# Kernel tuning notes

Measured on AMD Instinct MI355X. Metric: run time of the kernel, lower is better.

## Reference

```python
import jax, jax.numpy as jnp
import numpy as np

B, C, H, W, L = 2, 64, 48, 48, 48
GH, GW, GL = 24, 24, 24  # gating signal at half resolution


def setup_inputs() -> dict:
    key = jax.random.key(0)
    k = jax.random.split(key, 6)
    x = jax.random.normal(k[0], (B, C, H, W, L), dtype=jnp.float32)
    g = jax.random.normal(k[1], (B, C, GH, GW, GL), dtype=jnp.float32)
    s = 1.0 / np.sqrt(C)
    W1 = jax.random.normal(k[2], (C, C), dtype=jnp.float32) * s  # conv1 1x1x1 weight (out,in)
    b1 = jax.random.normal(k[3], (C,), dtype=jnp.float32) * 0.01
    W2 = jax.random.normal(k[4], (C, C), dtype=jnp.float32) * s  # conv2 1x1x1 weight
    b2 = jax.random.normal(k[5], (C,), dtype=jnp.float32) * 0.01
    return {"x": x, "g": g, "W1": W1, "b1": b1, "W2": W2, "b2": b2}


def _conv1x1(v, Wm, b):
    # 1x1x1 Conv3d == channel-mixing matmul
    return jnp.einsum('bchwl,oc->bohwl', v, Wm) + b[None, :, None, None, None]


def reference(x, g, W1, b1, W2, b2):
    theta_x = _conv1x1(x, W1, b1)                       # (B, C, H, W, L)
    theta_g = _conv1x1(g, W2, b2)                       # (B, C, GH, GW, GL)
    # F.upsample(mode='trilinear', align_corners=False) -> half-pixel trilinear resize
    theta_g = jax.image.resize(theta_g, (B, C, H, W, L), method='trilinear')

    # spatially-normalized elementwise gate
    theta_c = theta_x * theta_g
    theta_c = theta_c - jnp.min(theta_c)                # global min over whole tensor
    theta_c = theta_c / jnp.sum(theta_c, axis=(2, 3, 4), keepdims=True)
    p = theta_c * x

    # channel-channel attention per (b,h,w), contracting over L
    theta_c_d = jnp.einsum('bihwl,bjhwl->bhwij', theta_x, theta_g)  # (B,H,W,C,C)
    theta_c_d = theta_c_d - jnp.min(theta_c_d)
    theta_c_d = theta_c_d / jnp.sum(theta_c_d, axis=(1, 2, 3, 4), keepdims=True)
    d = jnp.einsum('bchwl,bhwcj->bjhwl', x, theta_c_d)  # (B, C, H, W, L)
    return (p, d)
```

## Files before the change

### kernel.cpp

```cpp
#include <hip/hip_runtime.h>

#define Bb 2
#define Cc 64
#define Hh 48
#define Ww 48
#define Ll 48
#define HWc (Hh*Ww)
#define HWL (HWc*Ll)
#define GHh 24
#define SG (GHh*GHh*GHh)
#define NBLK (Bb*HWc)
#define CNT1f 110592.0f
#define CNT2f 9437184.0f

__device__ __forceinline__ void interp1(int i, int& a, int& b, float& f){
  float src = i*0.5f - 0.25f;
  float fl = floorf(src);
  f = src - fl;
  int i0 = (int)fl;
  a = i0 < 0 ? 0 : i0;
  int i1 = i0 + 1;
  b = i1 > (GHh-1) ? (GHh-1) : i1;
}

__global__ __launch_bounds__(256) void conv_k(const float* __restrict__ in,
    const float* __restrict__ Wm, const float* __restrict__ bias,
    float* __restrict__ out, int S){
  __shared__ __align__(16) float Wl[64][68];
  __shared__ __align__(16) float xl[64][68];
  int t = threadIdx.x;
  int ntile = S >> 6;
  int b  = blockIdx.x / ntile;
  int s0 = (blockIdx.x % ntile) << 6;
  for (int q = t; q < 4096; q += 256){
    int o = q >> 6, c = q & 63;
    Wl[c][o] = Wm[q];
  }
  const float* inb = in + (size_t)b*Cc*S + s0;
  for (int q = t; q < 1024; q += 256){
    int c = q >> 4, v = (q & 15) << 2;
    float4 val = *(const float4*)(inb + (size_t)c*S + v);
    *(float4*)&xl[c][v] = val;
  }
  __syncthreads();
  int o0 = (t & 15) << 2, s1 = (t >> 4) << 2;
  float a00=0,a01=0,a02=0,a03=0,a10=0,a11=0,a12=0,a13=0;
  float a20=0,a21=0,a22=0,a23=0,a30=0,a31=0,a32=0,a33=0;
  #pragma unroll 8
  for (int c = 0; c < 64; ++c){
    float4 wv = *(const float4*)&Wl[c][o0];
    float4 xv = *(const float4*)&xl[c][s1];
    a00 += wv.x*xv.x; a01 += wv.x*xv.y; a02 += wv.x*xv.z; a03 += wv.x*xv.w;
    a10 += wv.y*xv.x; a11 += wv.y*xv.y; a12 += wv.y*xv.z; a13 += wv.y*xv.w;
    a20 += wv.z*xv.x; a21 += wv.z*xv.y; a22 += wv.z*xv.z; a23 += wv.z*xv.w;
    a30 += wv.w*xv.x; a31 += wv.w*xv.y; a32 += wv.w*xv.z; a33 += wv.w*xv.w;
  }
  float* ob = out + (size_t)b*Cc*S + s0 + s1;
  float b0 = bias[o0+0], b1v = bias[o0+1], b2v = bias[o0+2], b3 = bias[o0+3];
  { float4 r = make_float4(a00+b0,a01+b0,a02+b0,a03+b0); *(float4*)(ob + (size_t)(o0+0)*S) = r; }
  { float4 r = make_float4(a10+b1v,a11+b1v,a12+b1v,a13+b1v); *(float4*)(ob + (size_t)(o0+1)*S) = r; }
  { float4 r = make_float4(a20+b2v,a21+b2v,a22+b2v,a23+b2v); *(float4*)(ob + (size_t)(o0+2)*S) = r; }
  { float4 r = make_float4(a30+b3,a31+b3,a32+b3,a33+b3); *(float4*)(ob + (size_t)(o0+3)*S) = r; }
}

__global__ __launch_bounds__(256) void upsample_k(const float* __restrict__ tgh,
    float* __restrict__ tg){
  __shared__ float shm[2][24][25];
  int t = threadIdx.x;
  int bc = blockIdx.x / Hh;
  int h  = blockIdx.x % Hh;
  int ha, hb; float fh; interp1(h, ha, hb, fh);
  const float* src = tgh + (size_t)bc*SG;
  for (int q = t; q < 288; q += 256){
    int p = q / 144, rem = q % 144;
    int w_ = rem / 6, vl = (rem % 6) << 2;
    int hs = p ? hb : ha;
    float4 v = *(const float4*)(src + (size_t)hs*576 + w_*24 + vl);
    shm[p][w_][vl+0]=v.x; shm[p][w_][vl+1]=v.y; shm[p][w_][vl+2]=v.z; shm[p][w_][vl+3]=v.w;
  }
  __syncthreads();
  float* dst = tg + ((size_t)bc*Hh + h)*HWc;
  float omf = 1.f - fh;
  #pragma unroll
  for (int k = 0; k < 9; ++k){
    int idx = t + (k << 8);
    int w = idx / 48, l = idx % 48;
    int wa, wb; float fw; interp1(w, wa, wb, fw);
    int la, lb; float fl; interp1(l, la, lb, fl);
    float vaa = omf*shm[0][wa][la] + fh*shm[1][wa][la];
    float vab = omf*shm[0][wa][lb] + fh*shm[1][wa][lb];
    float vba = omf*shm[0][wb][la] + fh*shm[1][wb][la];
    float vbb = omf*shm[0][wb][lb] + fh*shm[1][wb][lb];
    float va = (1.f-fw)*vaa + fw*vba;
    float vb = (1.f-fw)*vab + fw*vbb;
    dst[idx] = (1.f-fl)*va + fl*vb;
  }
}

__global__ __launch_bounds__(256) void reduce_k(const float* __restrict__ tx,
    const float* __restrict__ tg, float* __restrict__ part_row,
    float* __restrict__ pm1, float* __restrict__ pm2, float* __restrict__ ps2){
  __shared__ __align__(16) float txt[48][68];
  __shared__ __align__(16) float tgt[48][68];
  __shared__ float red[512];
  __shared__ float sxg[48];
  int t = threadIdx.x;
  int bIdx = blockIdx.x;
  int b = bIdx / HWc, hw = bIdx % HWc;
  const float* txb = tx + ((size_t)b*Cc*HWc + hw)*Ll;
  const float* tgb = tg + ((size_t)b*Cc*HWc + hw)*Ll;
  for (int q = t; q < 768; q += 256){
    int c = q / 12, v = (q % 12) << 2;
    float4 a = *(const float4*)(txb + (size_t)c*HWL + v);
    txt[v+0][c]=a.x; txt[v+1][c]=a.y; txt[v+2][c]=a.z; txt[v+3][c]=a.w;
    float4 g = *(const float4*)(tgb + (size_t)c*HWL + v);
    tgt[v+0][c]=g.x; tgt[v+1][c]=g.y; tgt[v+2][c]=g.z; tgt[v+3][c]=g.w;
  }
  __syncthreads();
  int c = t & 63, lg = t >> 6;
  float psum = 0.f, pmin = 3.4e38f;
  #pragma unroll
  for (int li = 0; li < 12; ++li){
    int l = lg*12 + li;
    float prod = txt[l][c]*tgt[l][c];
    psum += prod;
    pmin = fminf(pmin, prod);
  }
  red[t] = psum;
  if (t < 48){
    float sx = 0.f, sg = 0.f;
    #pragma unroll 8
    for (int cc = 0; cc < 64; ++cc){ sx += txt[t][cc]; sg += tgt[t][cc]; }
    sxg[t] = sx*sg;
  }
  __syncthreads();
  if (t < 64) part_row[(size_t)bIdx*64 + t] = red[t]+red[t+64]+red[t+128]+red[t+192];
  int i0 = (t & 15) << 2, j0 = (t >> 4) << 2;
  float a00=0,a01=0,a02=0,a03=0,a10=0,a11=0,a12=0,a13=0;
  float a20=0,a21=0,a22=0,a23=0,a30=0,a31=0,a32=0,a33=0;
  #pragma unroll 4
  for (int l = 0; l < 48; ++l){
    float4 av = *(const float4*)&txt[l][i0];
    float4 bv = *(const float4*)&tgt[l][j0];
    a00 += av.x*bv.x; a01 += av.x*bv.y; a02 += av.x*bv.z; a03 += av.x*bv.w;
    a10 += av.y*bv.x; a11 += av.y*bv.y; a12 += av.y*bv.z; a13 += av.y*bv.w;
    a20 += av.z*bv.x; a21 += av.z*bv.y; a22 += av.z*bv.z; a23 += av.z*bv.w;
    a30 += av.w*bv.x; a31 += av.w*bv.y; a32 += av.w*bv.z; a33 += av.w*bv.w;
  }
  float amin = fminf(fminf(fminf(a00,a01),fminf(a02,a03)),
               fminf(fminf(fminf(a10,a11),fminf(a12,a13)),
               fminf(fminf(fminf(a20,a21),fminf(a22,a23)),
                     fminf(fminf(a30,a31),fminf(a32,a33)))));
  __syncthreads();
  red[t] = pmin; red[256+t] = amin;
  __syncthreads();
  if (t < 128){
    red[t] = fminf(red[t], red[t+128]);
    red[256+t] = fminf(red[256+t], red[256+t+128]);
  }
  __syncthreads();
  if (t < 64){
    float v1 = fminf(red[t], red[t+64]);
    float v2 = fminf(red[256+t], red[256+t+64]);
    #pragma unroll
    for (int off = 32; off; off >>= 1){
      v1 = fminf(v1, __shfl_down(v1, off));
      v2 = fminf(v2, __shfl_down(v2, off));
    }
    if (t == 0){
      pm1[bIdx] = v1; pm2[bIdx] = v2;
      float tot = 0.f;
      #pragma unroll
      for (int l = 0; l < 48; ++l) tot += sxg[l];
      ps2[bIdx] = tot;
    }
  }
}

__global__ __launch_bounds__(256) void reduce2_k(const float* __restrict__ part_row,
    const float* __restrict__ pm1, const float* __restrict__ pm2,
    const float* __restrict__ ps2, float* __restrict__ rowsum,
    float* __restrict__ gmin, float* __restrict__ s2v){
  __shared__ float red[512];
  int t = threadIdx.x, blk = blockIdx.x;
  if (blk < 128){
    int b = blk >> 6, c = blk & 63;
    const float* src = part_row + (size_t)b*HWc*64 + c;
    float s = 0.f;
    #pragma unroll
    for (int k = 0; k < 9; ++k){
      int i = t + (k << 8);
      s += src[(size_t)i*64];
    }
    red[t] = s; __syncthreads();
    for (int sgap = 128; sgap >= 64; sgap >>= 1){
      if (t < sgap) red[t] += red[t+sgap];
      __syncthreads();
    }
    if (t < 64){
      float v = red[t];
      #pragma unroll
      for (int off = 32; off; off >>= 1) v += __shfl_down(v, off);
      if (t == 0) rowsum[blk] = v;
    }
  } else if (blk == 128){
    float m1 = 3.4e38f, m2 = 3.4e38f;
    for (int i = t; i < NBLK; i += 256){ m1 = fminf(m1, pm1[i]); m2 = fminf(m2, pm2[i]); }
    red[t] = m1; red[256+t] = m2; __syncthreads();
    for (int s = 128; s >= 1; s >>= 1){
      if (t < s){ red[t] = fminf(red[t], red[t+s]); red[256+t] = fminf(red[256+t], red[256+t+s]); }
      __syncthreads();
    }
    if (t == 0){ gmin[0] = red[0]; gmin[1] = red[256]; }
  } else {
    float sa = 0.f, sb = 0.f;
    for (int i = t; i < HWc; i += 256){ sa += ps2[i]; sb += ps2[HWc + i]; }
    red[t] = sa; red[256+t] = sb; __syncthreads();
    for (int s = 128; s >= 1; s >>= 1){
      if (t < s){ red[t] += red[t+s]; red[256+t] += red[256+t+s]; }
      __syncthreads();
    }
    if (t == 0){ s2v[0] = red[0]; s2v[1] = red[256]; }
  }
}

__global__ __launch_bounds__(256) void final_k(const float* __restrict__ x,
    const float* __restrict__ tx, const float* __restrict__ tg,
    const float* __restrict__ gmin, const float* __restrict__ rowsum,
    const float* __restrict__ s2v, float* __restrict__ outp, float* __restrict__ outd){
  __shared__ __align__(16) float sh[6528 + 3328 + 48 + 64];
  float* txt = sh;
  float* tgt = sh + 3264;
  float* At  = sh;
  float* xs  = sh + 6528;
  float* Xs  = sh + 6528 + 3328;
  float* iv1 = Xs + 48;
  int t = threadIdx.x;
  int bIdx = blockIdx.x;
  int b = bIdx / HWc, hw = bIdx % HWc;
  size_t sbase = ((size_t)b*Cc*HWc + hw)*Ll;
  const float* txb = tx + sbase;
  const float* tgb = tg + sbase;
  const float* xb  = x  + sbase;
  for (int q = t; q < 768; q += 256){
    int c = q / 12, v = (q % 12) << 2;
    float4 a = *(const float4*)(txb + (size_t)c*HWL + v);
    txt[(v+0)*68+c]=a.x; txt[(v+1)*68+c]=a.y; txt[(v+2)*68+c]=a.z; txt[(v+3)*68+c]=a.w;
    float4 g = *(const float4*)(tgb + (size_t)c*HWL + v);
    tgt[(v+0)*68+c]=g.x; tgt[(v+1)*68+c]=g.y; tgt[(v+2)*68+c]=g.z; tgt[(v+3)*68+c]=g.w;
    float4 xv = *(const float4*)(xb + (size_t)c*HWL + v);
    *(float4*)&xs[c*52 + v] = xv;
  }
  __syncthreads();
  if (t < 48){
    float s = 0.f;
    #pragma unroll 8
    for (int cc = 0; cc < 64; ++cc) s += xs[cc*52 + t];
    Xs[t] = s;
  }
  float m1 = gmin[0], m2 = gmin[1];
  if (t < 64) iv1[t] = 1.f/(rowsum[b*64 + t] - m1*CNT1f);
  float invd2 = 1.f/(s2v[b] - m2*CNT2f);
  int i0 = (t & 15) << 2, j0 = (t >> 4) << 2;
  float a00=0,a01=0,a02=0,a03=0,a10=0,a11=0,a12=0,a13=0;
  float a20=0,a21=0,a22=0,a23=0,a30=0,a31=0,a32=0,a33=0;
  #pragma unroll 4
  for (int l = 0; l < 48; ++l){
    float4 av = *(const float4*)&txt[l*68 + i0];
    float4 bv = *(const float4*)&tgt[l*68 + j0];
    a00 += av.x*bv.x; a01 += av.x*bv.y; a02 += av.x*bv.z; a03 += av.x*bv.w;
    a10 += av.y*bv.x; a11 += av.y*bv.y; a12 += av.y*bv.z; a13 += av.y*bv.w;
    a20 += av.z*bv.x; a21 += av.z*bv.y; a22 += av.z*bv.z; a23 += av.z*bv.w;
    a30 += av.w*bv.x; a31 += av.w*bv.y; a32 += av.w*bv.z; a33 += av.w*bv.w;
  }
  __syncthreads();
  #pragma unroll
  for (int k = 0; k < 12; ++k){
    int e = t + (k << 8);
    int cc = e / 48, l = e % 48;
    float pv = (txt[l*68+cc]*tgt[l*68+cc] - m1)*iv1[cc]*xs[cc*52+l];
    outp[sbase + (size_t)cc*HWL + l] = pv;
  }
  __syncthreads();
  { float4 r = make_float4(a00,a01,a02,a03); *(float4*)&At[(i0+0)*68 + j0] = r; }
  { float4 r = make_float4(a10,a11,a12,a13); *(float4*)&At[(i0+1)*68 + j0] = r; }
  { float4 r = make_float4(a20,a21,a22,a23); *(float4*)&At[(i0+2)*68 + j0] = r; }
  { float4 r = make_float4(a30,a31,a32,a33); *(float4*)&At[(i0+3)*68 + j0] = r; }
  __syncthreads();
  if (t < 192){
    int jj = (t & 15) << 2, l0 = (t >> 4) << 2;
    float d00=0,d01=0,d02=0,d03=0,d10=0,d11=0,d12=0,d13=0;
    float d20=0,d21=0,d22=0,d23=0,d30=0,d31=0,d32=0,d33=0;
    #pragma unroll 4
    for (int cc = 0; cc < 64; ++cc){
      float4 av = *(const float4*)&At[cc*68 + jj];
      float4 xv = *(const float4*)&xs[cc*52 + l0];
      d00 += av.x*xv.x; d01 += av.x*xv.y; d02 += av.x*xv.z; d03 += av.x*xv.w;
      d10 += av.y*xv.x; d11 += av.y*xv.y; d12 += av.y*xv.z; d13 += av.y*xv.w;
      d20 += av.z*xv.x; d21 += av.z*xv.y; d22 += av.z*xv.z; d23 += av.z*xv.w;
      d30 += av.w*xv.x; d31 += av.w*xv.y; d32 += av.w*xv.z; d33 += av.w*xv.w;
    }
    float xs0 = m2*Xs[l0+0], xs1 = m2*Xs[l0+1], xs2 = m2*Xs[l0+2], xs3 = m2*Xs[l0+3];
    { float4 r = make_float4((d00-xs0)*invd2,(d01-xs1)*invd2,(d02-xs2)*invd2,(d03-xs3)*invd2);
      *(float4*)(outd + sbase + (size_t)(jj+0)*HWL + l0) = r; }
    { float4 r = make_float4((d10-xs0)*invd2,(d11-xs1)*invd2,(d12-xs2)*invd2,(d13-xs3)*invd2);
      *(float4*)(outd + sbase + (size_t)(jj+1)*HWL + l0) = r; }
    { float4 r = make_float4((d20-xs0)*invd2,(d21-xs1)*invd2,(d22-xs2)*invd2,(d23-xs3)*invd2);
      *(float4*)(outd + sbase + (size_t)(jj+2)*HWL + l0) = r; }
    { float4 r = make_float4((d30-xs0)*invd2,(d31-xs1)*invd2,(d32-xs2)*invd2,(d33-xs3)*invd2);
      *(float4*)(outd + sbase + (size_t)(jj+3)*HWL + l0) = r; }
  }
}

extern "C" void kernel_launch(void* const* d_in, const int* in_sizes, int n_in,
                              void* d_out, int out_size, void* d_ws, size_t ws_size,
                              hipStream_t stream){
  (void)in_sizes; (void)n_in; (void)out_size; (void)ws_size;
  const float* x  = (const float*)d_in[0];
  const float* g  = (const float*)d_in[1];
  const float* W1 = (const float*)d_in[2];
  const float* b1 = (const float*)d_in[3];
  const float* W2 = (const float*)d_in[4];
  const float* b2 = (const float*)d_in[5];
  float* outp = (float*)d_out;
  float* outd = outp + (size_t)Bb*Cc*HWL;
  float* ws   = (float*)d_ws;
  float* txw  = ws;
  float* tgw  = txw + (size_t)Bb*Cc*HWL;
  float* tghw = tgw + (size_t)Bb*Cc*HWL;
  float* part_row = tghw + (size_t)Bb*Cc*SG;
  float* pm1 = part_row + (size_t)NBLK*64;
  float* pm2 = pm1 + NBLK;
  float* ps2 = pm2 + NBLK;
  float* rowsum = ps2 + NBLK;
  float* gmin = rowsum + 128;
  float* s2v  = gmin + 2;

  hipLaunchKernelGGL(conv_k, dim3(Bb*(SG/64)), dim3(256), 0, stream, g, W2, b2, tghw, SG);
  hipLaunchKernelGGL(conv_k, dim3(Bb*(HWL/64)), dim3(256), 0, stream, x, W1, b1, txw, HWL);
  hipLaunchKernelGGL(upsample_k, dim3(Bb*Cc*Hh), dim3(256), 0, stream, tghw, tgw);
  hipLaunchKernelGGL(reduce_k, dim3(NBLK), dim3(256), 0, stream, txw, tgw, part_row, pm1, pm2, ps2);
  hipLaunchKernelGGL(reduce2_k, dim3(130), dim3(256), 0, stream, part_row, pm1, pm2, ps2, rowsum, gmin, s2v);
  hipLaunchKernelGGL(final_k, dim3(NBLK), dim3(256), 0, stream, x, txw, tgw, gmin, rowsum, s2v, outp, outd);
}
```

Baseline: 334.6 us.

## Fuse trilinear upsample into reduce kernel and compute p output during load

The reduce kernel now reads the low-resolution gate directly and performs trilinear interpolation in shared memory, so it no longer has to read the full-resolution upsampled tensor. The upsample kernel still runs, after reduce, because final_k needs it. In final_k the p output is computed from registers while tiles are loaded and written as float4, which removes a separate shared-memory pass and scalar stores. This adds more shared memory per block in reduce_k and extra interpolation arithmetic.

```diff
diff --git a/kernel.cpp b/kernel.cpp
--- a/kernel.cpp
+++ b/kernel.cpp
@@ -98,39 +98,62 @@
 }
 
 __global__ __launch_bounds__(256) void reduce_k(const float* __restrict__ tx,
-    const float* __restrict__ tg, float* __restrict__ part_row,
+    const float* __restrict__ tgh, float* __restrict__ part_row,
     float* __restrict__ pm1, float* __restrict__ pm2, float* __restrict__ ps2){
-  __shared__ __align__(16) float txt[48][68];
-  __shared__ __align__(16) float tgt[48][68];
-  __shared__ float red[512];
-  __shared__ float sxg[48];
+  __shared__ __align__(16) float txt[48*68];
+  __shared__ __align__(16) float tgt[48*68];
+  __shared__ __align__(16) float th2[64*53];
+  float* red = th2;
+  float* sxg = th2 + 512;
   int t = threadIdx.x;
   int bIdx = blockIdx.x;
   int b = bIdx / HWc, hw = bIdx % HWc;
+  int h = hw / Ww, w = hw % Ww;
+  int ha, hb; float fh; interp1(h, ha, hb, fh);
+  int wa, wb; float fw; interp1(w, wa, wb, fw);
   const float* txb = tx + ((size_t)b*Cc*HWc + hw)*Ll;
-  const float* tgb = tg + ((size_t)b*Cc*HWc + hw)*Ll;
   for (int q = t; q < 768; q += 256){
     int c = q / 12, v = (q % 12) << 2;
     float4 a = *(const float4*)(txb + (size_t)c*HWL + v);
-    txt[v+0][c]=a.x; txt[v+1][c]=a.y; txt[v+2][c]=a.z; txt[v+3][c]=a.w;
-    float4 g = *(const float4*)(tgb + (size_t)c*HWL + v);
-    tgt[v+0][c]=g.x; tgt[v+1][c]=g.y; tgt[v+2][c]=g.z; tgt[v+3][c]=g.w;
+    txt[(v+0)*68+c]=a.x; txt[(v+1)*68+c]=a.y; txt[(v+2)*68+c]=a.z; txt[(v+3)*68+c]=a.w;
+  }
+  float omfh = 1.f - fh;
+  for (int q = t; q < 768; q += 256){
+    int c = q / 12; int rem = q % 12; int ew = rem / 6; int v = (rem % 6) << 2;
+    int gw_ = ew ? wb : wa;
+    const float* pa = tgh + (((size_t)(b*Cc + c)*GHh + ha)*GHh + gw_)*GHh + v;
+    const float* pb = tgh + (((size_t)(b*Cc + c)*GHh + hb)*GHh + gw_)*GHh + v;
+    float4 A = *(const float4*)pa;
+    float4 Bv = *(const float4*)pb;
+    float* dst = &th2[c*53 + ew*26 + v];
+    dst[0] = omfh*A.x + fh*Bv.x;
+    dst[1] = omfh*A.y + fh*Bv.y;
+    dst[2] = omfh*A.z + fh*Bv.z;
+    dst[3] = omfh*A.w + fh*Bv.w;
   }
   __syncthreads();
   int c = t & 63, lg = t >> 6;
+  const float* thc = &th2[c*53];
   float psum = 0.f, pmin = 3.4e38f;
+  float omfw = 1.f - fw;
   #pragma unroll
   for (int li = 0; li < 12; ++li){
     int l = lg*12 + li;
-    float prod = txt[l][c]*tgt[l][c];
+    int la, lb; float fl; interp1(l, la, lb, fl);
+    float va = omfw*thc[la] + fw*thc[26+la];
+    float vb = omfw*thc[lb] + fw*thc[26+lb];
+    float tg = (1.f-fl)*va + fl*vb;
+    tgt[l*68+c] = tg;
+    float prod = txt[l*68+c]*tg;
     psum += prod;
     pmin = fminf(pmin, prod);
   }
+  __syncthreads();
   red[t] = psum;
   if (t < 48){
     float sx = 0.f, sg = 0.f;
     #pragma unroll 8
-    for (int cc = 0; cc < 64; ++cc){ sx += txt[t][cc]; sg += tgt[t][cc]; }
+    for (int cc = 0; cc < 64; ++cc){ sx += txt[t*68+cc]; sg += tgt[t*68+cc]; }
     sxg[t] = sx*sg;
   }
   __syncthreads();
@@ -140,8 +163,8 @@
   float a20=0,a21=0,a22=0,a23=0,a30=0,a31=0,a32=0,a33=0;
   #pragma unroll 4
   for (int l = 0; l < 48; ++l){
-    float4 av = *(const float4*)&txt[l][i0];
-    float4 bv = *(const float4*)&tgt[l][j0];
+    float4 av = *(const float4*)&txt[l*68 + i0];
+    float4 bv = *(const float4*)&tgt[l*68 + j0];
     a00 += av.x*bv.x; a01 += av.x*bv.y; a02 += av.x*bv.z; a03 += av.x*bv.w;
     a10 += av.y*bv.x; a11 += av.y*bv.y; a12 += av.y*bv.z; a13 += av.y*bv.w;
     a20 += av.z*bv.x; a21 += av.z*bv.y; a22 += av.z*bv.z; a23 += av.z*bv.w;
@@ -242,14 +265,25 @@
   const float* txb = tx + sbase;
   const float* tgb = tg + sbase;
   const float* xb  = x  + sbase;
+  float m1 = gmin[0], m2 = gmin[1];
+  if (t < 64) iv1[t] = 1.f/(rowsum[b*64 + t] - m1*CNT1f);
+  float invd2 = 1.f/(s2v[b] - m2*CNT2f);
+  __syncthreads();
   for (int q = t; q < 768; q += 256){
     int c = q / 12, v = (q % 12) << 2;
     float4 a = *(const float4*)(txb + (size_t)c*HWL + v);
+    float4 g = *(const float4*)(tgb + (size_t)c*HWL + v);
+    float4 xv = *(const float4*)(xb + (size_t)c*HWL + v);
     txt[(v+0)*68+c]=a.x; txt[(v+1)*68+c]=a.y; txt[(v+2)*68+c]=a.z; txt[(v+3)*68+c]=a.w;
-    float4 g = *(const float4*)(tgb + (size_t)c*HWL + v);
     tgt[(v+0)*68+c]=g.x; tgt[(v+1)*68+c]=g.y; tgt[(v+2)*68+c]=g.z; tgt[(v+3)*68+c]=g.w;
-    float4 xv = *(const float4*)(xb + (size_t)c*HWL + v);
     *(float4*)&xs[c*52 + v] = xv;
+    float ivc = iv1[c];
+    float4 pv;
+    pv.x = (a.x*g.x - m1)*ivc*xv.x;
+    pv.y = (a.y*g.y - m1)*ivc*xv.y;
+    pv.z = (a.z*g.z - m1)*ivc*xv.z;
+    pv.w = (a.w*g.w - m1)*ivc*xv.w;
+    *(float4*)(outp + sbase + (size_t)c*HWL + v) = pv;
   }
   __syncthreads();
   if (t < 48){
@@ -258,9 +292,6 @@
     for (int cc = 0; cc < 64; ++cc) s += xs[cc*52 + t];
     Xs[t] = s;
   }
-  float m1 = gmin[0], m2 = gmin[1];
-  if (t < 64) iv1[t] = 1.f/(rowsum[b*64 + t] - m1*CNT1f);
-  float invd2 = 1.f/(s2v[b] - m2*CNT2f);
   int i0 = (t & 15) << 2, j0 = (t >> 4) << 2;
   float a00=0,a01=0,a02=0,a03=0,a10=0,a11=0,a12=0,a13=0;
   float a20=0,a21=0,a22=0,a23=0,a30=0,a31=0,a32=0,a33=0;
@@ -272,14 +303,6 @@
     a10 += av.y*bv.x; a11 += av.y*bv.y; a12 += av.y*bv.z; a13 += av.y*bv.w;
     a20 += av.z*bv.x; a21 += av.z*bv.y; a22 += av.z*bv.z; a23 += av.z*bv.w;
     a30 += av.w*bv.x; a31 += av.w*bv.y; a32 += av.w*bv.z; a33 += av.w*bv.w;
-  }
-  __syncthreads();
-  #pragma unroll
-  for (int k = 0; k < 12; ++k){
-    int e = t + (k << 8);
-    int cc = e / 48, l = e % 48;
-    float pv = (txt[l*68+cc]*tgt[l*68+cc] - m1)*iv1[cc]*xs[cc*52+l];
-    outp[sbase + (size_t)cc*HWL + l] = pv;
   }
   __syncthreads();
   { float4 r = make_float4(a00,a01,a02,a03); *(float4*)&At[(i0+0)*68 + j0] = r; }
@@ -338,8 +361,8 @@
 
   hipLaunchKernelGGL(conv_k, dim3(Bb*(SG/64)), dim3(256), 0, stream, g, W2, b2, tghw, SG);
   hipLaunchKernelGGL(conv_k, dim3(Bb*(HWL/64)), dim3(256), 0, stream, x, W1, b1, txw, HWL);
+  hipLaunchKernelGGL(reduce_k, dim3(NBLK), dim3(256), 0, stream, txw, tghw, part_row, pm1, pm2, ps2);
   hipLaunchKernelGGL(upsample_k, dim3(Bb*Cc*Hh), dim3(256), 0, stream, tghw, tgw);
-  hipLaunchKernelGGL(reduce_k, dim3(NBLK), dim3(256), 0, stream, txw, tgw, part_row, pm1, pm2, ps2);
   hipLaunchKernelGGL(reduce2_k, dim3(130), dim3(256), 0, stream, part_row, pm1, pm2, ps2, rowsum, gmin, s2v);
   hipLaunchKernelGGL(final_k, dim3(NBLK), dim3(256), 0, stream, x, txw, tgw, gmin, rowsum, s2v, outp, outd);
 }
```

Result: slower. 346.9 us (+3.6%).
